# Kernel tuning notes

Measured on AMD Instinct MI355X. Metric: run time of the kernel, lower is better.

## Reference

```python
import jax, jax.numpy as jnp
import numpy as np

B, C = 4096, 128
EPS_BN = 1e-5  # torch BatchNorm1d default eps
EPS_ATT = 1e-9


def setup_inputs() -> dict:
    key = jax.random.key(0)
    ks = jax.random.split(key, 6)
    x1 = jax.random.normal(ks[0], (B, C, 1), jnp.float32)
    x2 = jax.random.normal(ks[1], (B, C, 1), jnp.float32)
    x1_2 = jax.random.normal(ks[2], (B, C, 1), jnp.float32)
    # trans_conv: Conv1d(C, C, kernel_size=1) -> weight (C_out, C_in)
    conv_w = jax.random.normal(ks[3], (C, C), jnp.float32) / np.sqrt(C).astype(np.float32)
    conv_b = jnp.zeros((C,), jnp.float32)
    # BatchNorm1d(C) affine params
    bn_gamma = jnp.ones((C,), jnp.float32)
    bn_beta = jnp.zeros((C,), jnp.float32)
    # fc_relation: Linear(2C+1, 1)
    fc_w = jax.random.normal(ks[4], (1, 2 * C + 1), jnp.float32) / np.sqrt(2 * C + 1).astype(np.float32)
    fc_b = jnp.zeros((1,), jnp.float32)
    return {"x1": x1, "x2": x2, "x1_2": x1_2, "conv_w": conv_w, "conv_b": conv_b,
            "bn_gamma": bn_gamma, "bn_beta": bn_beta, "fc_w": fc_w, "fc_b": fc_b}


def reference(x1, x2, x1_2, conv_w, conv_b, bn_gamma, bn_beta, fc_w, fc_b):
    # energy = bmm(x1, x2^T): (B,C,1) x (B,1,C) -> (B,C,C) outer product
    energy = jnp.einsum('bcl,bdl->bcd', x1, x2)
    energy = jax.nn.softmax(energy, axis=-1)
    # normalize columns (sum over dim=1)
    attention = energy / (EPS_ATT + energy.sum(axis=1, keepdims=True))
    # x_r = bmm(attention, x1_2): (B,C,C) x (B,C,1) -> (B,C,1)
    x_r = jnp.einsum('bcd,bdl->bcl', attention, x1_2)
    # 1x1 conv = per-position channel mixing
    t = jnp.einsum('oc,bcl->bol', conv_w, x_r) + conv_b[None, :, None]
    y = x1 - t
    # BatchNorm1d in training mode: per-channel stats over (batch, length)
    mean = y.mean(axis=(0, 2), keepdims=True)          # (1,C,1)
    var = y.var(axis=(0, 2), keepdims=True)            # biased variance
    y = (y - mean) * jax.lax.rsqrt(var + EPS_BN)
    y = y * bn_gamma[None, :, None] + bn_beta[None, :, None]
    x_r_out = jax.nn.relu(y)                            # (B,C,1)
    # gated fusion: cat([energy, energy^T, x1], dim=2) -> (B, C, 2C+1)
    feat = jnp.concatenate([energy, jnp.swapaxes(energy, 1, 2), x1], axis=2)
    gate = jax.nn.sigmoid(jnp.einsum('bcf,of->bco', feat, fc_w) + fc_b)  # (B,C,1)
    return gate * x1 + x_r_out
```

## Files before the change

### kernel.cpp

```cpp
#include <hip/hip_runtime.h>

#define B_ 4096
#define C_ 128
#define EPS_ATT 1e-9f
#define EPS_BN 1e-5f
#define LOG2E 1.44269504088896f

using short8 = __attribute__((ext_vector_type(8))) short;
using f32x4 = __attribute__((ext_vector_type(4))) float;
using u32x2 = __attribute__((ext_vector_type(2))) unsigned int;

__device__ __forceinline__ unsigned short bf16b(float x) {
    __bf16 h = (__bf16)x;
    return __builtin_bit_cast(unsigned short, h);
}

__global__ __launch_bounds__(256) void k_transpose(const float* __restrict__ W,
                                                   float* __restrict__ WT) {
    int j = blockIdx.x * 256 + threadIdx.x;
    if (j < C_ * C_) {
        int r = j >> 7;
        int col = j & (C_ - 1);
        WT[col * C_ + r] = W[j];
    }
}

__global__ __launch_bounds__(256, 4) void k_batch(
    const float* __restrict__ x1, const float* __restrict__ x2,
    const float* __restrict__ x12, const float* __restrict__ WT,
    const float* __restrict__ fcw, const float* __restrict__ fcb,
    const float* __restrict__ convb,
    float* __restrict__ Y, float* __restrict__ GX1) {
    const int b = blockIdx.x;
    const int tid = threadIdx.x;
    const int lane = tid & 63;
    const int w = tid >> 6;
    const int g = lane >> 4;
    const int ls = lane & 15;

    __shared__ char s_buf[C_ * C_ * 2] __attribute__((aligned(16)));
    __shared__ float s_x1[C_] __attribute__((aligned(16)));
    __shared__ float s_x2[C_] __attribute__((aligned(16)));
    __shared__ float s_fcC[C_] __attribute__((aligned(16)));
    __shared__ float s_invZ[C_] __attribute__((aligned(16)));
    __shared__ float s_cs4[4][C_] __attribute__((aligned(16)));
    __shared__ float s_s24[4][C_] __attribute__((aligned(16)));
    __shared__ float s_S1[C_] __attribute__((aligned(16)));
    __shared__ float s_xr[C_] __attribute__((aligned(16)));
    __shared__ unsigned short s_w3bf[C_] __attribute__((aligned(16)));
    __shared__ unsigned short s_f1bf[C_] __attribute__((aligned(16)));

    float v12 = 0.f, vcb = 0.f;
    if (tid < C_) {
        float v1 = x1[b * C_ + tid];
        s_x1[tid] = v1;
        s_x2[tid] = x2[b * C_ + tid];
        s_f1bf[tid] = bf16b(fcw[tid]);
        s_fcC[tid] = fcw[C_ + tid];
        v12 = x12[b * C_ + tid];
        vcb = convb[tid];
    }
    __syncthreads();

    short8 ef0[4], ef1[4];
    float zp0 = 0.f, zp1 = 0.f;
    {
        const float r0 = s_x1[32 * w + ls] * LOG2E;
        const float r1 = s_x1[32 * w + 16 + ls] * LOG2E;
        char* erow0 = s_buf + (32 * w + ls) * 256;
        char* erow1 = s_buf + (32 * w + 16 + ls) * 256;
        const int sw = (ls & 7) << 4;
#pragma unroll
        for (int q = 0; q < 4; ++q) {
            f32x4 xa = *(const f32x4*)&s_x2[32 * q + 8 * g];
            f32x4 xb = *(const f32x4*)&s_x2[32 * q + 8 * g + 4];
            union {
                short8 v;
                unsigned short u[8];
            } p0, p1;
#pragma unroll
            for (int j = 0; j < 4; ++j) {
                float a0 = __builtin_amdgcn_exp2f(r0 * xa[j]);
                float b0 = __builtin_amdgcn_exp2f(r0 * xb[j]);
                float a1 = __builtin_amdgcn_exp2f(r1 * xa[j]);
                float b1 = __builtin_amdgcn_exp2f(r1 * xb[j]);
                zp0 += a0 + b0;
                zp1 += a1 + b1;
                p0.u[j] = bf16b(a0);
                p0.u[j + 4] = bf16b(b0);
                p1.u[j] = bf16b(a1);
                p1.u[j + 4] = bf16b(b1);
            }
            ef0[q] = p0.v;
            ef1[q] = p1.v;
            const int off = (64 * q + 16 * g) ^ sw;
            *(short8*)(erow0 + off) = p0.v;
            *(short8*)(erow1 + off) = p1.v;
        }
    }
    zp0 += __shfl_xor(zp0, 16);
    zp0 += __shfl_xor(zp0, 32);
    zp1 += __shfl_xor(zp1, 16);
    zp1 += __shfl_xor(zp1, 32);
    if (lane < 16) {
        s_invZ[32 * w + ls] = 1.f / zp0;
        s_invZ[32 * w + 16 + ls] = 1.f / zp1;
    }
    __syncthreads();

    {
        const int grp = tid & 31;
        const int sl = tid >> 5;
        const char* eb = s_buf + sl * 16 * 256;
        const int octb = grp >> 1;
        const int hoff = (grp & 1) * 8;
        float cs[4] = {0.f, 0.f, 0.f, 0.f};
        float s2[4] = {0.f, 0.f, 0.f, 0.f};
#pragma unroll
        for (int k = 0; k < 4; ++k) {
            f32x4 iz4 = *(const f32x4*)&s_invZ[sl * 16 + 4 * k];
            f32x4 fc4 = *(const f32x4*)&s_fcC[sl * 16 + 4 * k];
#pragma unroll
            for (int rr = 0; rr < 4; ++rr) {
                const int r = 4 * k + rr;
                const float iz = iz4[rr];
                const float izf = iz * fc4[rr];
                u32x2 ev = *(const u32x2*)(eb + r * 256 +
                                           ((octb ^ (r & 7)) << 4) + hoff);
#pragma unroll
                for (int d = 0; d < 2; ++d) {
                    float elo = __builtin_bit_cast(float, ev[d] << 16);
                    float ehi =
                        __builtin_bit_cast(float, ev[d] & 0xffff0000u);
                    cs[2 * d] = fmaf(elo, iz, cs[2 * d]);
                    s2[2 * d] = fmaf(elo, izf, s2[2 * d]);
                    cs[2 * d + 1] = fmaf(ehi, iz, cs[2 * d + 1]);
                    s2[2 * d + 1] = fmaf(ehi, izf, s2[2 * d + 1]);
                }
            }
        }
#pragma unroll
        for (int k = 0; k < 4; ++k) {
            cs[k] += __shfl_xor(cs[k], 32);
            s2[k] += __shfl_xor(s2[k], 32);
        }
        if ((sl & 1) == 0) {
            f32x4 c4 = {cs[0], cs[1], cs[2], cs[3]};
            f32x4 t4 = {s2[0], s2[1], s2[2], s2[3]};
            *(f32x4*)&s_cs4[w][grp * 4] = c4;
            *(f32x4*)&s_s24[w][grp * 4] = t4;
        }
    }
    __syncthreads();

    if (tid < C_) {
        float cs = s_cs4[0][tid] + s_cs4[1][tid] + s_cs4[2][tid] + s_cs4[3][tid];
        float w3 = v12 / (EPS_ATT + cs);
        s_w3bf[tid] = bf16b(w3);
    }
    __syncthreads();

    {
        const short8 z8 = {0, 0, 0, 0, 0, 0, 0, 0};
        short8 bq[4];
#pragma unroll
        for (int q = 0; q < 4; ++q) {
            if (ls == 0)
                bq[q] = *(const short8*)&s_f1bf[q * 32 + g * 8];
            else if (ls == 1)
                bq[q] = *(const short8*)&s_w3bf[q * 32 + g * 8];
            else
                bq[q] = z8;
        }
        f32x4 acc0 = {0.f, 0.f, 0.f, 0.f};
        f32x4 acc1 = {0.f, 0.f, 0.f, 0.f};
#pragma unroll
        for (int q = 0; q < 4; ++q) {
            acc0 = __builtin_amdgcn_mfma_f32_16x16x32_bf16(ef0[q], bq[q], acc0, 0, 0, 0);
            acc1 = __builtin_amdgcn_mfma_f32_16x16x32_bf16(ef1[q], bq[q], acc1, 0, 0, 0);
        }
        if (ls < 2) {
            float* dst = ls ? s_xr : s_S1;
            *(f32x4*)&dst[(2 * w + 0) * 16 + g * 4] = acc0;
            *(f32x4*)&dst[(2 * w + 1) * 16 + g * 4] = acc1;
        }
    }
    __syncthreads();

    if (tid < C_) {
        float invz = s_invZ[tid];
        float S1 = s_S1[tid] * invz;
        float xr = s_xr[tid] * invz;
        float S2 = s_s24[0][tid] + s_s24[1][tid] + s_s24[2][tid] + s_s24[3][tid];
        s_xr[tid] = xr;
        float gg = S1 + S2 + s_x1[tid] * fcw[2 * C_] + fcb[0];
        float gate = 1.f / (1.f + __builtin_amdgcn_exp2f(-LOG2E * gg));
        GX1[b * C_ + tid] = gate * s_x1[tid];
    }
    __syncthreads();

    {
        const int quad = tid & 31;
        const int chunk = tid >> 5;
        f32x4 acc = {0.f, 0.f, 0.f, 0.f};
#pragma unroll
        for (int ii = 0; ii < 16; ++ii) {
            const int i = chunk * 16 + ii;
            const float x = s_xr[i];
            f32x4 wv = *(const f32x4*)&WT[i * C_ + quad * 4];
            acc[0] = fmaf(wv[0], x, acc[0]);
            acc[1] = fmaf(wv[1], x, acc[1]);
            acc[2] = fmaf(wv[2], x, acc[2]);
            acc[3] = fmaf(wv[3], x, acc[3]);
        }
        float* tp4 = (float*)s_buf;
        *(f32x4*)&tp4[chunk * C_ + quad * 4] = acc;
    }
    __syncthreads();

    if (tid < C_) {
        const float* tp4 = (const float*)s_buf;
        float t = vcb;
#pragma unroll
        for (int k = 0; k < 8; ++k) t += tp4[k * C_ + tid];
        Y[b * C_ + tid] = s_x1[tid] - t;
    }
}

__global__ __launch_bounds__(256) void k_pstat(const float* __restrict__ Y,
                                               float* __restrict__ pst) {
    const int slice = blockIdx.x;
    const int t = threadIdx.x;
    const f32x4* Yb = (const f32x4*)(Y + slice * 64 * C_);
    f32x4 s = {0.f, 0.f, 0.f, 0.f};
    f32x4 q = {0.f, 0.f, 0.f, 0.f};
#pragma unroll
    for (int p = 0; p < 8; ++p) {
        f32x4 y = Yb[p * 256 + t];
        s += y;
        q += y * y;
    }
    __shared__ f32x4 sh[256];
    __shared__ f32x4 sh2[256];
    sh[t] = s;
    sh2[t] = q;
    __syncthreads();
#pragma unroll
    for (int off = 128; off >= 32; off >>= 1) {
        if (t < off) {
            sh[t] += sh[t + off];
            sh2[t] += sh2[t + off];
        }
        __syncthreads();
    }
    if (t < 32) {
        f32x4 a = sh[t];
        f32x4 b2 = sh2[t];
#pragma unroll
        for (int j = 0; j < 4; ++j) {
            pst[(t * 4 + j) * 64 + slice] = a[j];
            pst[8192 + (t * 4 + j) * 64 + slice] = b2[j];
        }
    }
}

__global__ __launch_bounds__(256) void k_final(const float* __restrict__ Y,
                                               const float* __restrict__ pst,
                                               const float* __restrict__ gamma,
                                               const float* __restrict__ beta,
                                               float* __restrict__ out) {
    const int t = threadIdx.x;
    const int i4 = blockIdx.x * 256 + t;
    float4 y = ((const float4*)Y)[i4];
    float4 o = ((const float4*)out)[i4];
    __shared__ float sA[C_];
    __shared__ float sB[C_];
    if (t < C_) {
        f32x4 a = {0.f, 0.f, 0.f, 0.f};
        f32x4 b2 = {0.f, 0.f, 0.f, 0.f};
#pragma unroll
        for (int k = 0; k < 16; ++k) {
            a += *(const f32x4*)&pst[t * 64 + k * 4];
            b2 += *(const f32x4*)&pst[8192 + t * 64 + k * 4];
        }
        float s = (a[0] + a[1]) + (a[2] + a[3]);
        float q = (b2[0] + b2[1]) + (b2[2] + b2[3]);
        float mean = s * (1.f / (float)B_);
        float var = q * (1.f / (float)B_) - mean * mean;
        float A = gamma[t] * rsqrtf(var + EPS_BN);
        sA[t] = A;
        sB[t] = beta[t] - mean * A;
    }
    __syncthreads();
    const int ch = (i4 * 4) & (C_ - 1);
    o.x += fmaxf(y.x * sA[ch + 0] + sB[ch + 0], 0.f);
    o.y += fmaxf(y.y * sA[ch + 1] + sB[ch + 1], 0.f);
    o.z += fmaxf(y.z * sA[ch + 2] + sB[ch + 2], 0.f);
    o.w += fmaxf(y.w * sA[ch + 3] + sB[ch + 3], 0.f);
    ((float4*)out)[i4] = o;
}

extern "C" void kernel_launch(void* const* d_in, const int* in_sizes, int n_in,
                              void* d_out, int out_size, void* d_ws,
                              size_t ws_size, hipStream_t stream) {
    const float* x1 = (const float*)d_in[0];
    const float* x2 = (const float*)d_in[1];
    const float* x12 = (const float*)d_in[2];
    const float* convw = (const float*)d_in[3];
    const float* convb = (const float*)d_in[4];
    const float* gamma = (const float*)d_in[5];
    const float* beta = (const float*)d_in[6];
    const float* fcw = (const float*)d_in[7];
    const float* fcb = (const float*)d_in[8];
    float* out = (float*)d_out;

    float* WT = (float*)d_ws;
    float* Y = WT + C_ * C_;
    float* pst = Y + (size_t)B_ * C_;

    k_transpose<<<(C_ * C_ + 255) / 256, 256, 0, stream>>>(convw, WT);
    k_batch<<<B_, 256, 0, stream>>>(x1, x2, x12, WT, fcw, fcb, convb, Y, out);
    k_pstat<<<64, 256, 0, stream>>>(Y, pst);
    k_final<<<(B_ * C_ / 4) / 256, 256, 0, stream>>>(Y, pst, gamma, beta, out);
}
```

Before: 42.52 us.

## Split conv into batched kernel reusing W in LDS, fuse BN partial stats

Moves the 1x1 conv out of the per-batch kernel into a new kernel that loads the weight matrix once into swizzled shared memory and applies it to 16 batch rows per block. Per-channel partial sums and sums of squares are computed in that same kernel, which removes the separate stats pass, and the transpose kernel is dropped. The final kernel uses 1024-thread blocks and reduces 256 partials. This trades per-batch global W reads for an extra XR round trip through global memory, and the new conv kernel runs only 256 blocks with 512 threads each and a large shared-memory footprint.

```diff
diff --git a/kernel.cpp b/kernel.cpp
--- a/kernel.cpp
+++ b/kernel.cpp
@@ -15,22 +15,11 @@
     return __builtin_bit_cast(unsigned short, h);
 }
 
-__global__ __launch_bounds__(256) void k_transpose(const float* __restrict__ W,
-                                                   float* __restrict__ WT) {
-    int j = blockIdx.x * 256 + threadIdx.x;
-    if (j < C_ * C_) {
-        int r = j >> 7;
-        int col = j & (C_ - 1);
-        WT[col * C_ + r] = W[j];
-    }
-}
-
 __global__ __launch_bounds__(256, 4) void k_batch(
     const float* __restrict__ x1, const float* __restrict__ x2,
-    const float* __restrict__ x12, const float* __restrict__ WT,
+    const float* __restrict__ x12,
     const float* __restrict__ fcw, const float* __restrict__ fcb,
-    const float* __restrict__ convb,
-    float* __restrict__ Y, float* __restrict__ GX1) {
+    float* __restrict__ XR, float* __restrict__ GX1) {
     const int b = blockIdx.x;
     const int tid = threadIdx.x;
     const int lane = tid & 63;
@@ -45,20 +34,19 @@
     __shared__ float s_invZ[C_] __attribute__((aligned(16)));
     __shared__ float s_cs4[4][C_] __attribute__((aligned(16)));
     __shared__ float s_s24[4][C_] __attribute__((aligned(16)));
-    __shared__ float s_S1[C_] __attribute__((aligned(16)));
-    __shared__ float s_xr[C_] __attribute__((aligned(16)));
-    __shared__ unsigned short s_w3bf[C_] __attribute__((aligned(16)));
     __shared__ unsigned short s_f1bf[C_] __attribute__((aligned(16)));
 
-    float v12 = 0.f, vcb = 0.f;
+    float* s_S1 = (float*)s_buf;
+    float* s_xrr = (float*)(s_buf + 512);
+    unsigned short* s_w3bf = (unsigned short*)(s_buf + 1024);
+
+    float v12 = 0.f;
     if (tid < C_) {
-        float v1 = x1[b * C_ + tid];
-        s_x1[tid] = v1;
+        s_x1[tid] = x1[b * C_ + tid];
         s_x2[tid] = x2[b * C_ + tid];
         s_f1bf[tid] = bf16b(fcw[tid]);
         s_fcC[tid] = fcw[C_ + tid];
         v12 = x12[b * C_ + tid];
-        vcb = convb[tid];
     }
     __syncthreads();
 
@@ -180,7 +168,7 @@
             acc1 = __builtin_amdgcn_mfma_f32_16x16x32_bf16(ef1[q], bq[q], acc1, 0, 0, 0);
         }
         if (ls < 2) {
-            float* dst = ls ? s_xr : s_S1;
+            float* dst = ls ? s_xrr : s_S1;
             *(f32x4*)&dst[(2 * w + 0) * 16 + g * 4] = acc0;
             *(f32x4*)&dst[(2 * w + 1) * 16 + g * 4] = acc1;
         }
@@ -190,109 +178,140 @@
     if (tid < C_) {
         float invz = s_invZ[tid];
         float S1 = s_S1[tid] * invz;
-        float xr = s_xr[tid] * invz;
+        float xr = s_xrr[tid] * invz;
         float S2 = s_s24[0][tid] + s_s24[1][tid] + s_s24[2][tid] + s_s24[3][tid];
-        s_xr[tid] = xr;
+        XR[b * C_ + tid] = xr;
         float gg = S1 + S2 + s_x1[tid] * fcw[2 * C_] + fcb[0];
         float gate = 1.f / (1.f + __builtin_amdgcn_exp2f(-LOG2E * gg));
         GX1[b * C_ + tid] = gate * s_x1[tid];
     }
-    __syncthreads();
-
-    {
-        const int quad = tid & 31;
-        const int chunk = tid >> 5;
+}
+
+__global__ __launch_bounds__(512, 2) void k_conv(
+    const float* __restrict__ W, const float* __restrict__ XR,
+    const float* __restrict__ x1, const float* __restrict__ convb,
+    float* __restrict__ Y, float* __restrict__ pst) {
+    const int blk = blockIdx.x;
+    const int tid = threadIdx.x;
+    const int bb = blk * 16;
+
+    __shared__ float s_W[C_ * C_] __attribute__((aligned(16)));
+    __shared__ float s_xr[16 * C_] __attribute__((aligned(16)));
+    __shared__ float s_tp[2 * 16 * C_] __attribute__((aligned(16)));
+
+#pragma unroll
+    for (int k = 0; k < 32; ++k) {
+        int j = k * 512 + tid;
+        int o = j >> 7, i = j & 127;
+        s_W[i * C_ + (o ^ (i & 28))] = W[j];
+    }
+#pragma unroll
+    for (int k = 0; k < 4; ++k) {
+        int j = k * 512 + tid;
+        s_xr[j] = XR[bb * C_ + j];
+    }
+    __syncthreads();
+
+    const int q = tid & 31;
+    const int sub = (tid >> 5) & 7;
+    const int ih = tid >> 8;
+    const int bl0 = 2 * sub, bl1 = bl0 + 1;
+    {
+        f32x4 a0 = {0.f, 0.f, 0.f, 0.f};
+        f32x4 a1 = {0.f, 0.f, 0.f, 0.f};
+#pragma unroll
+        for (int iq = 0; iq < 16; ++iq) {
+            const int i0 = ih * 64 + 4 * iq;
+            f32x4 xv0 = *(const f32x4*)&s_xr[bl0 * C_ + i0];
+            f32x4 xv1 = *(const f32x4*)&s_xr[bl1 * C_ + i0];
+#pragma unroll
+            for (int u = 0; u < 4; ++u) {
+                const int i = i0 + u;
+                f32x4 wv = *(const f32x4*)&s_W[i * C_ + ((4 * q) ^ (i & 28))];
+                a0[0] = fmaf(wv[0], xv0[u], a0[0]);
+                a0[1] = fmaf(wv[1], xv0[u], a0[1]);
+                a0[2] = fmaf(wv[2], xv0[u], a0[2]);
+                a0[3] = fmaf(wv[3], xv0[u], a0[3]);
+                a1[0] = fmaf(wv[0], xv1[u], a1[0]);
+                a1[1] = fmaf(wv[1], xv1[u], a1[1]);
+                a1[2] = fmaf(wv[2], xv1[u], a1[2]);
+                a1[3] = fmaf(wv[3], xv1[u], a1[3]);
+            }
+        }
+        *(f32x4*)&s_tp[(ih * 16 + bl0) * C_ + 4 * q] = a0;
+        *(f32x4*)&s_tp[(ih * 16 + bl1) * C_ + 4 * q] = a1;
+    }
+    __syncthreads();
+
+    float* s_sa = s_W;
+    float* s_sb = s_W + 16 * C_;
+    {
+        const int bl = tid >> 5;
+        const int gb = bb + bl;
+        f32x4 t4 = *(const f32x4*)&s_tp[bl * C_ + 4 * q];
+        f32x4 t4b = *(const f32x4*)&s_tp[(16 + bl) * C_ + 4 * q];
+        f32x4 cb = *(const f32x4*)&convb[4 * q];
+        f32x4 xv = *(const f32x4*)&x1[gb * C_ + 4 * q];
+        f32x4 y;
+#pragma unroll
+        for (int u = 0; u < 4; ++u) y[u] = xv[u] - (t4[u] + t4b[u] + cb[u]);
+        *(f32x4*)&Y[gb * C_ + 4 * q] = y;
+        *(f32x4*)&s_sa[bl * C_ + 4 * q] = y;
+        f32x4 y2;
+#pragma unroll
+        for (int u = 0; u < 4; ++u) y2[u] = y[u] * y[u];
+        *(f32x4*)&s_sb[bl * C_ + 4 * q] = y2;
+    }
+    __syncthreads();
+
+    if (tid < 64) {
+        const int qq = tid & 31;
+        const float* src = (tid < 32) ? s_sa : s_sb;
         f32x4 acc = {0.f, 0.f, 0.f, 0.f};
 #pragma unroll
-        for (int ii = 0; ii < 16; ++ii) {
-            const int i = chunk * 16 + ii;
-            const float x = s_xr[i];
-            f32x4 wv = *(const f32x4*)&WT[i * C_ + quad * 4];
-            acc[0] = fmaf(wv[0], x, acc[0]);
-            acc[1] = fmaf(wv[1], x, acc[1]);
-            acc[2] = fmaf(wv[2], x, acc[2]);
-            acc[3] = fmaf(wv[3], x, acc[3]);
-        }
-        float* tp4 = (float*)s_buf;
-        *(f32x4*)&tp4[chunk * C_ + quad * 4] = acc;
-    }
-    __syncthreads();
-
-    if (tid < C_) {
-        const float* tp4 = (const float*)s_buf;
-        float t = vcb;
-#pragma unroll
-        for (int k = 0; k < 8; ++k) t += tp4[k * C_ + tid];
-        Y[b * C_ + tid] = s_x1[tid] - t;
-    }
-}
-
-__global__ __launch_bounds__(256) void k_pstat(const float* __restrict__ Y,
-                                               float* __restrict__ pst) {
-    const int slice = blockIdx.x;
+        for (int bl = 0; bl < 16; ++bl)
+            acc += *(const f32x4*)&src[bl * C_ + 4 * qq];
+        float* dst = pst + (tid < 32 ? 0 : C_ * 256);
+#pragma unroll
+        for (int j = 0; j < 4; ++j) dst[(4 * qq + j) * 256 + blk] = acc[j];
+    }
+}
+
+__global__ __launch_bounds__(1024) void k_final(const float* __restrict__ Y,
+                                                const float* __restrict__ pst,
+                                                const float* __restrict__ gamma,
+                                                const float* __restrict__ beta,
+                                                float* __restrict__ out) {
     const int t = threadIdx.x;
-    const f32x4* Yb = (const f32x4*)(Y + slice * 64 * C_);
-    f32x4 s = {0.f, 0.f, 0.f, 0.f};
-    f32x4 q = {0.f, 0.f, 0.f, 0.f};
-#pragma unroll
-    for (int p = 0; p < 8; ++p) {
-        f32x4 y = Yb[p * 256 + t];
-        s += y;
-        q += y * y;
-    }
-    __shared__ f32x4 sh[256];
-    __shared__ f32x4 sh2[256];
-    sh[t] = s;
-    sh2[t] = q;
-    __syncthreads();
-#pragma unroll
-    for (int off = 128; off >= 32; off >>= 1) {
-        if (t < off) {
-            sh[t] += sh[t + off];
-            sh2[t] += sh2[t + off];
-        }
-        __syncthreads();
-    }
-    if (t < 32) {
-        f32x4 a = sh[t];
-        f32x4 b2 = sh2[t];
-#pragma unroll
-        for (int j = 0; j < 4; ++j) {
-            pst[(t * 4 + j) * 64 + slice] = a[j];
-            pst[8192 + (t * 4 + j) * 64 + slice] = b2[j];
-        }
-    }
-}
-
-__global__ __launch_bounds__(256) void k_final(const float* __restrict__ Y,
-                                               const float* __restrict__ pst,
-                                               const float* __restrict__ gamma,
-                                               const float* __restrict__ beta,
-                                               float* __restrict__ out) {
-    const int t = threadIdx.x;
-    const int i4 = blockIdx.x * 256 + t;
+    const int i4 = blockIdx.x * 1024 + t;
     float4 y = ((const float4*)Y)[i4];
     float4 o = ((const float4*)out)[i4];
+
+    __shared__ float s_red[2][4][C_];
     __shared__ float sA[C_];
     __shared__ float sB[C_];
+    {
+        const int ch = t & 127;
+        const int seg = (t >> 7) & 3;
+        const int arr = t >> 9;
+        const float* src = pst + arr * (C_ * 256) + ch * 256 + seg * 64;
+        f32x4 a = {0.f, 0.f, 0.f, 0.f};
+#pragma unroll
+        for (int k = 0; k < 16; ++k) a += *(const f32x4*)&src[4 * k];
+        s_red[arr][seg][ch] = (a[0] + a[1]) + (a[2] + a[3]);
+    }
+    __syncthreads();
     if (t < C_) {
-        f32x4 a = {0.f, 0.f, 0.f, 0.f};
-        f32x4 b2 = {0.f, 0.f, 0.f, 0.f};
-#pragma unroll
-        for (int k = 0; k < 16; ++k) {
-            a += *(const f32x4*)&pst[t * 64 + k * 4];
-            b2 += *(const f32x4*)&pst[8192 + t * 64 + k * 4];
-        }
-        float s = (a[0] + a[1]) + (a[2] + a[3]);
-        float q = (b2[0] + b2[1]) + (b2[2] + b2[3]);
+        float s = s_red[0][0][t] + s_red[0][1][t] + s_red[0][2][t] + s_red[0][3][t];
+        float qv = s_red[1][0][t] + s_red[1][1][t] + s_red[1][2][t] + s_red[1][3][t];
         float mean = s * (1.f / (float)B_);
-        float var = q * (1.f / (float)B_) - mean * mean;
+        float var = qv * (1.f / (float)B_) - mean * mean;
         float A = gamma[t] * rsqrtf(var + EPS_BN);
         sA[t] = A;
         sB[t] = beta[t] - mean * A;
     }
     __syncthreads();
-    const int ch = (i4 * 4) & (C_ - 1);
+    const int ch = (4 * t) & (C_ - 1);
     o.x += fmaxf(y.x * sA[ch + 0] + sB[ch + 0], 0.f);
     o.y += fmaxf(y.y * sA[ch + 1] + sB[ch + 1], 0.f);
     o.z += fmaxf(y.z * sA[ch + 2] + sB[ch + 2], 0.f);
@@ -314,12 +333,11 @@
     const float* fcb = (const float*)d_in[8];
     float* out = (float*)d_out;
 
-    float* WT = (float*)d_ws;
-    float* Y = WT + C_ * C_;
+    float* XR = (float*)d_ws;
+    float* Y = XR + (size_t)B_ * C_;
     float* pst = Y + (size_t)B_ * C_;
 
-    k_transpose<<<(C_ * C_ + 255) / 256, 256, 0, stream>>>(convw, WT);
-    k_batch<<<B_, 256, 0, stream>>>(x1, x2, x12, WT, fcw, fcb, convb, Y, out);
-    k_pstat<<<64, 256, 0, stream>>>(Y, pst);
-    k_final<<<(B_ * C_ / 4) / 256, 256, 0, stream>>>(Y, pst, gamma, beta, out);
-}
+    k_batch<<<B_, 256, 0, stream>>>(x1, x2, x12, fcw, fcb, XR, out);
+    k_conv<<<256, 512, 0, stream>>>(convw, XR, x1, convb, Y, pst);
+    k_final<<<(B_ * C_ / 4) / 1024, 1024, 0, stream>>>(Y, pst, gamma, beta, out);
+}
```

Result: faster. 40.48 us (-4.8%).
